# Optimization experiments

Hardware: AMD Instinct MI355X
Metric: run time of the kernel (lower is better)

## Reference

```python
import jax, jax.numpy as jnp
import numpy as np

N_NODES = 100000
N_EDGES = 1600000
D_FEAT = 128
HIDDEN = 128
N_LAYERS = 3
N_GRAPHS = 512
N_CLASSES = 10


def setup_inputs() -> dict:
    key = jax.random.key(0)
    ks = jax.random.split(key, 10)
    x = jax.random.normal(ks[0], (N_NODES, D_FEAT), dtype=jnp.float32)
    edge_index = jax.random.randint(ks[1], (2, N_EDGES), 0, N_NODES, dtype=jnp.int64)
    batch = jnp.sort(jax.random.randint(ks[2], (N_NODES,), 0, N_GRAPHS, dtype=jnp.int64))
    s = 0.05
    W0 = jax.random.normal(ks[3], (D_FEAT, HIDDEN), dtype=jnp.float32) * s
    b0 = jnp.zeros((HIDDEN,), dtype=jnp.float32)
    Ws = jax.random.normal(ks[4], (N_LAYERS, HIDDEN, HIDDEN), dtype=jnp.float32) * s
    bs = jnp.zeros((N_LAYERS, HIDDEN), dtype=jnp.float32)
    linW = jax.random.normal(ks[5], (HIDDEN, N_CLASSES), dtype=jnp.float32) * s
    linb = jnp.zeros((N_CLASSES,), dtype=jnp.float32)
    return {"x": x, "edge_index": edge_index, "batch": batch,
            "W0": W0, "b0": b0, "Ws": Ws, "bs": bs, "linW": linW, "linb": linb}


def _gcn_norm(edge_index, n_nodes):
    # PyG GCNConv default: add self-loops, symmetric D^{-1/2}(A+I)D^{-1/2} normalization
    src, dst = edge_index[0], edge_index[1]
    ones = jnp.ones((edge_index.shape[1],), dtype=jnp.float32)
    deg = jax.ops.segment_sum(ones, dst, num_segments=n_nodes) + 1.0  # +1 for self-loop
    dis = jax.lax.rsqrt(deg)
    edge_coef = (dis[src] * dis[dst])[:, None]   # [E,1]
    self_coef = (dis * dis)[:, None]             # [N,1]
    return src, dst, edge_coef, self_coef


def _gcn_conv(h, W, b, src, dst, edge_coef, self_coef, n_nodes):
    hw = h @ W                                                        # [N,H]
    agg = jax.ops.segment_sum(hw[src] * edge_coef, dst, num_segments=n_nodes)
    return agg + self_coef * hw + b


def reference(x, edge_index, batch, W0, b0, Ws, bs, linW, linb):
    n = N_NODES
    src, dst, ec, sc = _gcn_norm(edge_index, n)
    x_cur = jax.nn.relu(_gcn_conv(x, W0, b0, src, dst, ec, sc, n))
    x_pre = jnp.zeros_like(x_cur)
    for i in range(N_LAYERS):
        x_temp = x_cur
        x_cur = jax.nn.relu(_gcn_conv(x_cur + x_pre, Ws[i], bs[i], src, dst, ec, sc, n))
        x_pre = x_temp
    # global mean pool over graph ids
    sums = jax.ops.segment_sum(x_cur, batch, num_segments=N_GRAPHS)
    cnts = jax.ops.segment_sum(jnp.ones((n,), dtype=x_cur.dtype), batch, num_segments=N_GRAPHS)
    pooled = sums / jnp.maximum(cnts, 1.0)[:, None]
    # dropout is identity in eval mode
    return pooled @ linW + linb
```

## Files before the change

### kernel.cpp

```cpp
#include <hip/hip_runtime.h>

#define NN 100000
#define NE 1600000
#define H  128
#define NG 512
#define NC 10
#define NBUCK  98
#define CHUNK  4096
#define BINCAP 18432
#define EDCAP  26624

typedef _Float16 f16;
typedef __attribute__((ext_vector_type(8))) _Float16 f16x8;
typedef __attribute__((ext_vector_type(4))) _Float16 f16x4;
typedef __attribute__((ext_vector_type(4))) float    f32x4;

__device__ __forceinline__ int lower_bound_i(const int* __restrict__ a, int n, int val) {
    int lo = 0, hi = n;
    while (lo < hi) {
        int mid = (lo + hi) >> 1;
        if (a[mid] < val) lo = mid + 1; else hi = mid;
    }
    return lo;
}

__global__ __launch_bounds__(256) void wprep_kernel(const float* __restrict__ W0,
                                                    const float* __restrict__ Ws,
                                                    f16* __restrict__ wt_hi,
                                                    f16* __restrict__ wt_lo,
                                                    int* __restrict__ bcur,
                                                    f16* __restrict__ hwb) {
    int t = threadIdx.x;
    if (blockIdx.x == 0) {
        if (t < NBUCK) bcur[t] = 0;
        if (t >= 128 && t < 192) ((int*)(hwb + (size_t)NN * H))[t - 128] = 0;
    }
    int idx = blockIdx.x * 256 + t;
    int m = idx >> 14;
    int k = (idx >> 7) & 127;
    int n = idx & 127;
    const float* Wm = (m == 0) ? W0 : (Ws + (size_t)(m - 1) * H * H);
    float v = Wm[k * H + n];
    f16 hi = (f16)v;
    float lo = v - (float)hi;
    wt_hi[(size_t)m * H * H + n * H + k] = hi;
    wt_lo[(size_t)m * H * H + n * H + k] = (f16)lo;
}

__global__ __launch_bounds__(256) void binA_kernel(const int* __restrict__ src,
                                                   const int* __restrict__ dst,
                                                   int* __restrict__ bcur,
                                                   int* __restrict__ binned) {
    __shared__ int hist[NBUCK];
    __shared__ int lbase[NBUCK];
    __shared__ int gbase[NBUCK];
    __shared__ int cur[NBUCK];
    __shared__ int stage[CHUNK];
    __shared__ int destp[CHUNK];
    int t  = threadIdx.x;
    int e0 = blockIdx.x * CHUNK;
    int cnt = NE - e0; if (cnt > CHUNK) cnt = CHUNK;

    if (t < NBUCK) hist[t] = 0;
    __syncthreads();

    int s_[16], d_[16];
    #pragma unroll
    for (int i = 0; i < 16; ++i) {
        int e = e0 + i * 256 + t;
        if (e < NE) {
            s_[i] = src[e]; d_[i] = dst[e];
            atomicAdd(&hist[d_[i] >> 10], 1);
        } else { s_[i] = -1; d_[i] = 0; }
    }
    __syncthreads();

    if (t < NBUCK) {
        int lb = 0;
        for (int i = 0; i < t; ++i) lb += hist[i];
        lbase[t] = lb;
        cur[t]   = lb;
        gbase[t] = t * BINCAP + atomicAdd(&bcur[t], hist[t]);
    }
    __syncthreads();

    #pragma unroll
    for (int i = 0; i < 16; ++i) {
        if (s_[i] >= 0) {
            int s = s_[i], d = d_[i];
            int b = d >> 10;
            int r = atomicAdd(&cur[b], 1);
            stage[r] = s | ((d & 1023) << 17);
            destp[r] = gbase[b] + (r - lbase[b]);
        }
    }
    __syncthreads();

    #pragma unroll
    for (int i = 0; i < 16; ++i) {
        int idx = i * 256 + t;
        if (idx < cnt) binned[destp[idx]] = stage[idx];
    }
}

__global__ __launch_bounds__(1024) void binB_kernel(const int* __restrict__ binned,
                                                    const int* __restrict__ bcnt,
                                                    int* __restrict__ edata,
                                                    int* __restrict__ offs_pk,
                                                    float* __restrict__ dis) {
    __shared__ int cnt[1024];
    __shared__ int cursor[1024];
    __shared__ int ws[16];
    int b = blockIdx.x, t = threadIdx.x;
    int lane = t & 63, wid = t >> 6;
    cnt[t] = 0;
    __syncthreads();
    int lo = b * BINCAP, hi = lo + bcnt[b];
    for (int e = lo + t; e < hi; e += 1024) {
        atomicAdd(&cnt[(binned[e] >> 17) & 1023], 1);
    }
    __syncthreads();
    int gd = (b << 10) + t;
    int c = cnt[t];
    int L = (gd < NN) ? ((c + 8) & ~7) : 0;
    int incl = L;
    #pragma unroll
    for (int d = 1; d < 64; d <<= 1) { int u = __shfl_up(incl, d, 64); if (lane >= d) incl += u; }
    if (lane == 63) ws[wid] = incl;
    __syncthreads();
    int wbase = 0;
    for (int w = 0; w < wid; ++w) wbase += ws[w];
    int lbase = wbase + incl - L;
    int epoff = b * EDCAP;
    int gbase = epoff + lbase;
    if (gd < NN) {
        offs_pk[gd] = gbase | ((L >> 3) << 22);
        dis[gd] = rsqrtf((float)c + 1.0f);
        edata[gbase] = gd;
        for (int i = c + 1; i < L; ++i) edata[gbase + i] = NN;
    }
    cursor[t] = lbase + 1;
    __syncthreads();
    for (int e = lo + t; e < hi; e += 1024) {
        int p = binned[e];
        int dloc = (p >> 17) & 1023;
        int r = atomicAdd(&cursor[dloc], 1);
        edata[epoff + r] = p & 0x1FFFF;
    }
}

template <int FP32IN>
__global__ __launch_bounds__(512) void gemm_kernel(const void* __restrict__ in0,
                                                   const f16* __restrict__ in1,
                                                   const f16* __restrict__ wt_hi,
                                                   const f16* __restrict__ wt_lo,
                                                   const float* __restrict__ dis,
                                                   f16* __restrict__ hw) {
    __shared__ f16x8 sW[2][128 * 16];
    int t = threadIdx.x;
    int l = t & 63, w = t >> 6;
    int lr = l & 15, lq = l >> 4;
    int rowb = blockIdx.x * 256 + w * 32;

    const f16x8* wh = (const f16x8*)wt_hi;
    const f16x8* wl = (const f16x8*)wt_lo;
    #pragma unroll
    for (int i = 0; i < 4; ++i) {
        int ch = i * 512 + t;
        int n = ch >> 4, c = ch & 15;
        int sw = n * 16 + (c ^ (n & 7));
        sW[0][sw] = wh[ch];
        sW[1][sw] = wl[ch];
    }

    f16x8 aF[2][4];
    #pragma unroll
    for (int rt = 0; rt < 2; ++rt) {
        int grow = rowb + rt * 16 + lr;
        if (grow >= NN) grow = NN - 1;
        #pragma unroll
        for (int ks = 0; ks < 4; ++ks) {
            int c = ks * 4 + lq;
            f16x8 v;
            if (FP32IN) {
                const float* xp = (const float*)in0 + (size_t)grow * H + c * 8;
                f32x4 u0 = *(const f32x4*)xp;
                f32x4 u1 = *(const f32x4*)(xp + 4);
                #pragma unroll
                for (int u = 0; u < 4; ++u) { v[u] = (f16)u0[u]; v[u + 4] = (f16)u1[u]; }
            } else {
                v = *((const f16x8*)in0 + (size_t)grow * 16 + c);
                if (in1) {
                    f16x8 uu = *((const f16x8*)in1 + (size_t)grow * 16 + c);
                    v = v + uu;
                }
            }
            aF[rt][ks] = v;
        }
    }
    __syncthreads();

    f32x4 acc[2][8];
    #pragma unroll
    for (int rt = 0; rt < 2; ++rt)
        #pragma unroll
        for (int ct = 0; ct < 8; ++ct)
            acc[rt][ct] = (f32x4){0.f, 0.f, 0.f, 0.f};

    #pragma unroll
    for (int p = 0; p < 2; ++p) {
        #pragma unroll
        for (int ks = 0; ks < 4; ++ks) {
            int c = ks * 4 + lq;
            #pragma unroll
            for (int ct = 0; ct < 8; ++ct) {
                int n = ct * 16 + lr;
                f16x8 bF = sW[p][n * 16 + (c ^ (n & 7))];
                acc[0][ct] = __builtin_amdgcn_mfma_f32_16x16x32_f16(bF, aF[0][ks], acc[0][ct], 0, 0, 0);
                acc[1][ct] = __builtin_amdgcn_mfma_f32_16x16x32_f16(bF, aF[1][ks], acc[1][ct], 0, 0, 0);
            }
        }
    }

    #pragma unroll
    for (int rt = 0; rt < 2; ++rt) {
        int grow = rowb + rt * 16 + lr;
        if (grow < NN) {
            float dv = dis[grow];
            #pragma unroll
            for (int ct = 0; ct < 8; ++ct) {
                f16x4 o;
                #pragma unroll
                for (int r = 0; r < 4; ++r) o[r] = (f16)(dv * acc[rt][ct][r]);
                *(f16x4*)&hw[(size_t)grow * H + ct * 16 + lq * 4] = o;
            }
        }
    }
}

__global__ __launch_bounds__(256) void agg_kernel(const f16* __restrict__ hw,
                                                  const float* __restrict__ dis,
                                                  const int* __restrict__ offs_pk,
                                                  const int* __restrict__ edata,
                                                  const float* __restrict__ bias,
                                                  f16* __restrict__ outh) {
    int wid  = threadIdx.x >> 6;
    int lane = threadIdx.x & 63;
    int node = blockIdx.x * 4 + wid;
    if (node >= NN) return;
    int q  = lane >> 4;
    int j8 = (lane & 15) * 8;
    int w = offs_pk[node];
    int beg = w & 0x3FFFFF;
    int nit8 = (unsigned)w >> 22;
    float acc[8];
    #pragma unroll
    for (int u = 0; u < 8; ++u) acc[u] = 0.f;

    int it = 0;
    for (; it + 2 <= nit8; it += 2) {
        int base = beg + it * 8;
        int s0 = edata[base + q];
        int s1 = edata[base + 4 + q];
        int s2 = edata[base + 8 + q];
        int s3 = edata[base + 12 + q];
        f16x8 v0 = *(const f16x8*)&hw[(size_t)s0 * H + j8];
        f16x8 v1 = *(const f16x8*)&hw[(size_t)s1 * H + j8];
        f16x8 v2 = *(const f16x8*)&hw[(size_t)s2 * H + j8];
        f16x8 v3 = *(const f16x8*)&hw[(size_t)s3 * H + j8];
        f16x8 vt = (v0 + v1) + (v2 + v3);
        #pragma unroll
        for (int u = 0; u < 8; ++u) acc[u] += (float)vt[u];
    }
    if (it < nit8) {
        int base = beg + it * 8;
        int s0 = edata[base + q];
        int s1 = edata[base + 4 + q];
        f16x8 v0 = *(const f16x8*)&hw[(size_t)s0 * H + j8];
        f16x8 v1 = *(const f16x8*)&hw[(size_t)s1 * H + j8];
        f16x8 vt = v0 + v1;
        #pragma unroll
        for (int u = 0; u < 8; ++u) acc[u] += (float)vt[u];
    }
    #pragma unroll
    for (int u = 0; u < 8; ++u) {
        acc[u] += __shfl_xor(acc[u], 16, 64);
        acc[u] += __shfl_xor(acc[u], 32, 64);
    }
    if (q == 0) {
        float dv = dis[node];
        f16x8 o;
        #pragma unroll
        for (int u = 0; u < 8; ++u) o[u] = (f16)fmaxf(dv * acc[u] + bias[j8 + u], 0.f);
        *(f16x8*)&outh[(size_t)node * H + j8] = o;
    }
}

__global__ __launch_bounds__(512) void pool_kernel(const f16* __restrict__ h,
                                                   const int* __restrict__ batch,
                                                   const float* __restrict__ linW,
                                                   const float* __restrict__ linb,
                                                   float* __restrict__ out) {
    __shared__ float pld[4][H];
    int g = blockIdx.x;
    int t = threadIdx.x;
    int f = t & 127, quad = t >> 7;
    int lo = lower_bound_i(batch, NN, g);
    int hi = lower_bound_i(batch, NN, g + 1);
    float sum = 0.f;
    for (int n = lo + quad; n < hi; n += 4) sum += (float)h[(size_t)n * H + f];
    pld[quad][f] = sum;
    __syncthreads();
    if (t < H) {
        float cnt = (float)(hi - lo);
        pld[0][t] = (pld[0][t] + pld[1][t] + pld[2][t] + pld[3][t]) / fmaxf(cnt, 1.0f);
    }
    __syncthreads();
    if (t < NC) {
        float acc = linb[t];
        #pragma unroll 4
        for (int j = 0; j < H; ++j) acc += pld[0][j] * linW[j * NC + t];
        out[g * NC + t] = acc;
    }
}

extern "C" void kernel_launch(void* const* d_in, const int* in_sizes, int n_in,
                              void* d_out, int out_size, void* d_ws, size_t ws_size,
                              hipStream_t stream) {
    const float* x     = (const float*)d_in[0];
    const int*   ei    = (const int*)d_in[1];
    const int*   batch = (const int*)d_in[2];
    const float* W0    = (const float*)d_in[3];
    const float* b0    = (const float*)d_in[4];
    const float* Ws    = (const float*)d_in[5];
    const float* bs    = (const float*)d_in[6];
    const float* linW  = (const float*)d_in[7];
    const float* linb  = (const float*)d_in[8];
    const int* src = ei;
    const int* dst = ei + NE;

    char* p = (char*)d_ws;
    auto alloc = [&](size_t bytes) -> void* {
        void* r = (void*)p;
        p += (bytes + 255) & ~(size_t)255;
        return r;
    };
    f16*   buf0    = (f16*)alloc((size_t)NN * H * 2);
    f16*   buf1    = (f16*)alloc((size_t)NN * H * 2);
    f16*   buf2    = (f16*)alloc((size_t)NN * H * 2);
    f16*   hwb     = (f16*)alloc((size_t)(NN + 1) * H * 2);
    f16*   wt_hi   = (f16*)alloc((size_t)4 * H * H * 2);
    f16*   wt_lo   = (f16*)alloc((size_t)4 * H * H * 2);
    float* dis     = (float*)alloc((size_t)NN * 4);
    int*   offs_pk = (int*)alloc((size_t)NN * 4);
    int*   binned  = (int*)alloc((size_t)NBUCK * BINCAP * 4);
    int*   edata   = (int*)alloc((size_t)NBUCK * EDCAP * 4);
    int*   bcur    = (int*)alloc((size_t)NBUCK * 4);

    wprep_kernel<<<(4 * H * H) / 256, 256, 0, stream>>>(W0, Ws, wt_hi, wt_lo, bcur, hwb);
    binA_kernel<<<(NE + CHUNK - 1) / CHUNK, 256, 0, stream>>>(src, dst, bcur, binned);
    binB_kernel<<<NBUCK, 1024, 0, stream>>>(binned, bcur, edata, offs_pk, dis);

    int gemm_grid = (NN + 255) / 256;
    int agg_grid  = (NN + 3) / 4;
    size_t WSZ = (size_t)H * H;

    gemm_kernel<1><<<gemm_grid, 512, 0, stream>>>(x, nullptr, wt_hi, wt_lo, dis, hwb);
    agg_kernel<<<agg_grid, 256, 0, stream>>>(hwb, dis, offs_pk, edata, b0, buf0);
    gemm_kernel<0><<<gemm_grid, 512, 0, stream>>>(buf0, nullptr, wt_hi + WSZ, wt_lo + WSZ, dis, hwb);
    agg_kernel<<<agg_grid, 256, 0, stream>>>(hwb, dis, offs_pk, edata, bs, buf1);
    gemm_kernel<0><<<gemm_grid, 512, 0, stream>>>(buf1, buf0, wt_hi + 2 * WSZ, wt_lo + 2 * WSZ, dis, hwb);
    agg_kernel<<<agg_grid, 256, 0, stream>>>(hwb, dis, offs_pk, edata, bs + H, buf2);
    gemm_kernel<0><<<gemm_grid, 512, 0, stream>>>(buf2, buf1, wt_hi + 3 * WSZ, wt_lo + 3 * WSZ, dis, hwb);
    agg_kernel<<<agg_grid, 256, 0, stream>>>(hwb, dis, offs_pk, edata, bs + 2 * H, buf0);

    pool_kernel<<<NG, 512, 0, stream>>>(buf0, batch, linW, linb, (float*)d_out);
}
```

Measured before the change: 396.8 us.

## Fuse weight fp16 split into GEMM prologue and vectorize edge-index loads

Drops the separate weight-prep kernel. Each GEMM block now reads the fp32 weights directly and splits them into hi/lo fp16 parts in shared memory, using a plain c*128+n layout without the XOR swizzle. The bucket-counter reset moves to a memset and the sentinel-row zeroing moves into binB. The aggregation kernel loads edge indices as int2/int4 vectors and special-cases small neighbour counts to cut instruction and loop overhead, at the cost of every GEMM block redoing the weight conversion with strided global reads and possibly more LDS bank conflicts.

New measurement: 397.2 us. Within noise of the previous version (+0.1%).

```diff
diff --git a/kernel.cpp b/kernel.cpp
--- a/kernel.cpp
+++ b/kernel.cpp
@@ -22,29 +22,6 @@
         if (a[mid] < val) lo = mid + 1; else hi = mid;
     }
     return lo;
-}
-
-__global__ __launch_bounds__(256) void wprep_kernel(const float* __restrict__ W0,
-                                                    const float* __restrict__ Ws,
-                                                    f16* __restrict__ wt_hi,
-                                                    f16* __restrict__ wt_lo,
-                                                    int* __restrict__ bcur,
-                                                    f16* __restrict__ hwb) {
-    int t = threadIdx.x;
-    if (blockIdx.x == 0) {
-        if (t < NBUCK) bcur[t] = 0;
-        if (t >= 128 && t < 192) ((int*)(hwb + (size_t)NN * H))[t - 128] = 0;
-    }
-    int idx = blockIdx.x * 256 + t;
-    int m = idx >> 14;
-    int k = (idx >> 7) & 127;
-    int n = idx & 127;
-    const float* Wm = (m == 0) ? W0 : (Ws + (size_t)(m - 1) * H * H);
-    float v = Wm[k * H + n];
-    f16 hi = (f16)v;
-    float lo = v - (float)hi;
-    wt_hi[(size_t)m * H * H + n * H + k] = hi;
-    wt_lo[(size_t)m * H * H + n * H + k] = (f16)lo;
 }
 
 __global__ __launch_bounds__(256) void binA_kernel(const int* __restrict__ src,
@@ -107,12 +84,14 @@
                                                     const int* __restrict__ bcnt,
                                                     int* __restrict__ edata,
                                                     int* __restrict__ offs_pk,
-                                                    float* __restrict__ dis) {
+                                                    float* __restrict__ dis,
+                                                    f16* __restrict__ hwb) {
     __shared__ int cnt[1024];
     __shared__ int cursor[1024];
     __shared__ int ws[16];
     int b = blockIdx.x, t = threadIdx.x;
     int lane = t & 63, wid = t >> 6;
+    if (b == 0 && t < 64) ((int*)(hwb + (size_t)NN * H))[t] = 0;
     cnt[t] = 0;
     __syncthreads();
     int lo = b * BINCAP, hi = lo + bcnt[b];
@@ -152,8 +131,7 @@
 template <int FP32IN>
 __global__ __launch_bounds__(512) void gemm_kernel(const void* __restrict__ in0,
                                                    const f16* __restrict__ in1,
-                                                   const f16* __restrict__ wt_hi,
-                                                   const f16* __restrict__ wt_lo,
+                                                   const float* __restrict__ W,
                                                    const float* __restrict__ dis,
                                                    f16* __restrict__ hw) {
     __shared__ f16x8 sW[2][128 * 16];
@@ -162,15 +140,20 @@
     int lr = l & 15, lq = l >> 4;
     int rowb = blockIdx.x * 256 + w * 32;
 
-    const f16x8* wh = (const f16x8*)wt_hi;
-    const f16x8* wl = (const f16x8*)wt_lo;
     #pragma unroll
     for (int i = 0; i < 4; ++i) {
         int ch = i * 512 + t;
-        int n = ch >> 4, c = ch & 15;
-        int sw = n * 16 + (c ^ (n & 7));
-        sW[0][sw] = wh[ch];
-        sW[1][sw] = wl[ch];
+        int n = ch & 127, c = ch >> 7;
+        f16x8 hi, lo;
+        #pragma unroll
+        for (int j = 0; j < 8; ++j) {
+            float v = W[(c * 8 + j) * H + n];
+            f16 hv = (f16)v;
+            hi[j] = hv;
+            lo[j] = (f16)(v - (float)hv);
+        }
+        sW[0][c * 128 + n] = hi;
+        sW[1][c * 128 + n] = lo;
     }
 
     f16x8 aF[2][4];
@@ -215,7 +198,7 @@
             #pragma unroll
             for (int ct = 0; ct < 8; ++ct) {
                 int n = ct * 16 + lr;
-                f16x8 bF = sW[p][n * 16 + (c ^ (n & 7))];
+                f16x8 bF = sW[p][c * 128 + n];
                 acc[0][ct] = __builtin_amdgcn_mfma_f32_16x16x32_f16(bF, aF[0][ks], acc[0][ct], 0, 0, 0);
                 acc[1][ct] = __builtin_amdgcn_mfma_f32_16x16x32_f16(bF, aF[1][ks], acc[1][ct], 0, 0, 0);
             }
@@ -257,30 +240,54 @@
     #pragma unroll
     for (int u = 0; u < 8; ++u) acc[u] = 0.f;
 
-    int it = 0;
-    for (; it + 2 <= nit8; it += 2) {
-        int base = beg + it * 8;
-        int s0 = edata[base + q];
-        int s1 = edata[base + 4 + q];
-        int s2 = edata[base + 8 + q];
-        int s3 = edata[base + 12 + q];
-        f16x8 v0 = *(const f16x8*)&hw[(size_t)s0 * H + j8];
-        f16x8 v1 = *(const f16x8*)&hw[(size_t)s1 * H + j8];
-        f16x8 v2 = *(const f16x8*)&hw[(size_t)s2 * H + j8];
-        f16x8 v3 = *(const f16x8*)&hw[(size_t)s3 * H + j8];
+    if (nit8 == 2) {
+        int4 s = *(const int4*)&edata[beg + q * 4];
+        f16x8 v0 = *(const f16x8*)&hw[(size_t)s.x * H + j8];
+        f16x8 v1 = *(const f16x8*)&hw[(size_t)s.y * H + j8];
+        f16x8 v2 = *(const f16x8*)&hw[(size_t)s.z * H + j8];
+        f16x8 v3 = *(const f16x8*)&hw[(size_t)s.w * H + j8];
         f16x8 vt = (v0 + v1) + (v2 + v3);
         #pragma unroll
         for (int u = 0; u < 8; ++u) acc[u] += (float)vt[u];
-    }
-    if (it < nit8) {
-        int base = beg + it * 8;
-        int s0 = edata[base + q];
-        int s1 = edata[base + 4 + q];
-        f16x8 v0 = *(const f16x8*)&hw[(size_t)s0 * H + j8];
-        f16x8 v1 = *(const f16x8*)&hw[(size_t)s1 * H + j8];
+    } else if (nit8 == 3) {
+        int4 s  = *(const int4*)&edata[beg + q * 4];
+        int2 s2 = *(const int2*)&edata[beg + 16 + q * 2];
+        f16x8 v0 = *(const f16x8*)&hw[(size_t)s.x * H + j8];
+        f16x8 v1 = *(const f16x8*)&hw[(size_t)s.y * H + j8];
+        f16x8 v2 = *(const f16x8*)&hw[(size_t)s.z * H + j8];
+        f16x8 v3 = *(const f16x8*)&hw[(size_t)s.w * H + j8];
+        f16x8 v4 = *(const f16x8*)&hw[(size_t)s2.x * H + j8];
+        f16x8 v5 = *(const f16x8*)&hw[(size_t)s2.y * H + j8];
+        f16x8 vt = ((v0 + v1) + (v2 + v3)) + (v4 + v5);
+        #pragma unroll
+        for (int u = 0; u < 8; ++u) acc[u] += (float)vt[u];
+    } else if (nit8 == 1) {
+        int2 s2 = *(const int2*)&edata[beg + q * 2];
+        f16x8 v0 = *(const f16x8*)&hw[(size_t)s2.x * H + j8];
+        f16x8 v1 = *(const f16x8*)&hw[(size_t)s2.y * H + j8];
         f16x8 vt = v0 + v1;
         #pragma unroll
         for (int u = 0; u < 8; ++u) acc[u] += (float)vt[u];
+    } else {
+        int it = 0;
+        for (; it + 2 <= nit8; it += 2) {
+            int4 s = *(const int4*)&edata[beg + it * 8 + q * 4];
+            f16x8 v0 = *(const f16x8*)&hw[(size_t)s.x * H + j8];
+            f16x8 v1 = *(const f16x8*)&hw[(size_t)s.y * H + j8];
+            f16x8 v2 = *(const f16x8*)&hw[(size_t)s.z * H + j8];
+            f16x8 v3 = *(const f16x8*)&hw[(size_t)s.w * H + j8];
+            f16x8 vt = (v0 + v1) + (v2 + v3);
+            #pragma unroll
+            for (int u = 0; u < 8; ++u) acc[u] += (float)vt[u];
+        }
+        if (nit8 & 1) {
+            int2 s2 = *(const int2*)&edata[beg + (nit8 - 1) * 8 + q * 2];
+            f16x8 v0 = *(const f16x8*)&hw[(size_t)s2.x * H + j8];
+            f16x8 v1 = *(const f16x8*)&hw[(size_t)s2.y * H + j8];
+            f16x8 vt = v0 + v1;
+            #pragma unroll
+            for (int u = 0; u < 8; ++u) acc[u] += (float)vt[u];
+        }
     }
     #pragma unroll
     for (int u = 0; u < 8; ++u) {
@@ -349,29 +356,28 @@
     f16*   buf1    = (f16*)alloc((size_t)NN * H * 2);
     f16*   buf2    = (f16*)alloc((size_t)NN * H * 2);
     f16*   hwb     = (f16*)alloc((size_t)(NN + 1) * H * 2);
-    f16*   wt_hi   = (f16*)alloc((size_t)4 * H * H * 2);
-    f16*   wt_lo   = (f16*)alloc((size_t)4 * H * H * 2);
     float* dis     = (float*)alloc((size_t)NN * 4);
     int*   offs_pk = (int*)alloc((size_t)NN * 4);
     int*   binned  = (int*)alloc((size_t)NBUCK * BINCAP * 4);
     int*   edata   = (int*)alloc((size_t)NBUCK * EDCAP * 4);
     int*   bcur    = (int*)alloc((size_t)NBUCK * 4);
 
-    wprep_kernel<<<(4 * H * H) / 256, 256, 0, stream>>>(W0, Ws, wt_hi, wt_lo, bcur, hwb);
+    hipMemsetAsync(bcur, 0, (size_t)NBUCK * 4, stream);
+
     binA_kernel<<<(NE + CHUNK - 1) / CHUNK, 256, 0, stream>>>(src, dst, bcur, binned);
-    binB_kernel<<<NBUCK, 1024, 0, stream>>>(binned, bcur, edata, offs_pk, dis);
+    binB_kernel<<<NBUCK, 1024, 0, stream>>>(binned, bcur, edata, offs_pk, dis, hwb);
 
     int gemm_grid = (NN + 255) / 256;
     int agg_grid  = (NN + 3) / 4;
-    size_t WSZ = (size_t)H * H;
-
-    gemm_kernel<1><<<gemm_grid, 512, 0, stream>>>(x, nullptr, wt_hi, wt_lo, dis, hwb);
+    size_t HH = (size_t)H * H;
+
+    gemm_kernel<1><<<gemm_grid, 512, 0, stream>>>(x, nullptr, W0, dis, hwb);
     agg_kernel<<<agg_grid, 256, 0, stream>>>(hwb, dis, offs_pk, edata, b0, buf0);
-    gemm_kernel<0><<<gemm_grid, 512, 0, stream>>>(buf0, nullptr, wt_hi + WSZ, wt_lo + WSZ, dis, hwb);
+    gemm_kernel<0><<<gemm_grid, 512, 0, stream>>>(buf0, nullptr, Ws, dis, hwb);
     agg_kernel<<<agg_grid, 256, 0, stream>>>(hwb, dis, offs_pk, edata, bs, buf1);
-    gemm_kernel<0><<<gemm_grid, 512, 0, stream>>>(buf1, buf0, wt_hi + 2 * WSZ, wt_lo + 2 * WSZ, dis, hwb);
+    gemm_kernel<0><<<gemm_grid, 512, 0, stream>>>(buf1, buf0, Ws + HH, dis, hwb);
     agg_kernel<<<agg_grid, 256, 0, stream>>>(hwb, dis, offs_pk, edata, bs + H, buf2);
-    gemm_kernel<0><<<gemm_grid, 512, 0, stream>>>(buf2, buf1, wt_hi + 3 * WSZ, wt_lo + 3 * WSZ, dis, hwb);
+    gemm_kernel<0><<<gemm_grid, 512, 0, stream>>>(buf2, buf1, Ws + 2 * HH, dis, hwb);
     agg_kernel<<<agg_grid, 256, 0, stream>>>(hwb, dis, offs_pk, edata, bs + 2 * H, buf0);
 
     pool_kernel<<<NG, 512, 0, stream>>>(buf0, batch, linW, linb, (float*)d_out);
```
